# Kernel tuning notes

Measured on AMD Instinct MI355X. Metric: run time of the kernel, lower is better.

Reference implementation:

```python
import jax, jax.numpy as jnp
import numpy as np
import math

IN_CH = 256
EMBED = 128


def setup_inputs() -> dict:
    key = jax.random.key(0)
    k1, k2, k3, k4, k5 = jax.random.split(key, 5)
    N, C, H, W = 4, IN_CH, 64, 64
    x = jax.random.normal(k1, (N, C, H, W), dtype=jnp.float32)
    # conv1x1 weights stored as [out_ch, in_ch] (kernel is 1x1)
    W_qkv = jax.random.normal(k2, (3 * EMBED, C), dtype=jnp.float32) * (1.0 / math.sqrt(C))
    b_qkv = jax.random.normal(k3, (3 * EMBED,), dtype=jnp.float32) * 0.01
    W_out = jax.random.normal(k4, (C, EMBED), dtype=jnp.float32) * (1.0 / math.sqrt(EMBED))
    b_out = jax.random.normal(k5, (C,), dtype=jnp.float32) * 0.01
    return {"x": x, "W_qkv": W_qkv, "b_qkv": b_qkv, "W_out": W_out, "b_out": b_out}


def reference(x, W_qkv, b_qkv, W_out, b_out):
    N, C, H, W = x.shape
    E = EMBED
    HW = H * W
    # conv1x1 QKV projection: (N, 3E, H, W)
    qkv = jnp.einsum('nchw,oc->nohw', x, W_qkv) + b_qkv[None, :, None, None]
    # faithful RAW C-order reshape (N, 3E, H, W) -> (N, HW, 3E), as in torch .reshape
    qkv = qkv.reshape(N, HW, 3 * E)
    q, k, v = jnp.split(qkv, 3, axis=-1)  # each (N, HW, E)
    # scores scaled by 1/sqrt(H*W), softmax over dim=-2 (columns)
    scores = jnp.einsum('nid,njd->nij', q, k) / math.sqrt(HW)
    soft = jax.nn.softmax(scores, axis=-2)
    out = jnp.einsum('nij,njd->nid', soft, v)  # (N, HW, E)
    # faithful RAW C-order reshape (N, HW, E) -> (N, E, H, W)
    out = out.reshape(N, E, H, W)
    # conv1x1 output projection
    y = jnp.einsum('nehw,ce->nchw', out, W_out) + b_out[None, :, None, None]
    return y
```

## Files before the change

kernel.cpp:

```cpp
#include <hip/hip_runtime.h>
#include <hip/hip_bf16.h>


typedef short bfrag __attribute__((ext_vector_type(8)));
typedef float ffrag __attribute__((ext_vector_type(4)));
typedef unsigned short us4 __attribute__((ext_vector_type(4)));
#define MFMA(a,b,c) __builtin_amdgcn_mfma_f32_16x16x32_bf16((a),(b),(c),0,0,0)

__device__ __forceinline__ unsigned short f2bf(float f){
  union { float f; unsigned u; } v; v.f = f;
  unsigned r = v.u + 0x7fffu + ((v.u >> 16) & 1u);
  return (unsigned short)(r >> 16);
}
__device__ __forceinline__ float bf2f(unsigned short h){
  union { unsigned u; float f; } v; v.u = ((unsigned)h) << 16; return v.f;
}
__device__ __forceinline__ unsigned bfpack(float a, float b){
  return (unsigned)f2bf(a) | ((unsigned)f2bf(b) << 16);
}

__global__ __launch_bounds__(256) void k_wcast(const float* __restrict__ Wq, const float* __restrict__ Wo,
                                               unsigned short* __restrict__ Wqb, unsigned short* __restrict__ Wob){
  int i = blockIdx.x*256 + threadIdx.x;
  if (i < 384*256) Wqb[i] = f2bf(Wq[i]);
  if (i < 256*128) Wob[i] = f2bf(Wo[i]);
}

__global__ __launch_bounds__(256) void k_qkv(const float* __restrict__ x, const unsigned short* __restrict__ Wqb,
                                             const float* __restrict__ bq, unsigned short* __restrict__ qkv){
  constexpr int LD = 136;
  __shared__ __align__(16) unsigned short As[64*LD];
  __shared__ __align__(16) unsigned short Bs[64*LD];
  const int o0 = blockIdx.x*64, h0 = blockIdx.y*64, n = blockIdx.z;
  const int t = threadIdx.x, w = t>>6, lane = t&63, lr = lane&15, q4 = lane>>4;
  ffrag acc[4] = {};
  for (int kh = 0; kh < 2; ++kh) {
    __syncthreads();
    #pragma unroll
    for (int r=0;r<4;++r){
      int pi = t + 256*r; int o = pi>>4, seg = pi&15;
      *(uint4*)&As[o*LD + seg*8] = *(const uint4*)(Wqb + (o0+o)*256 + kh*128 + seg*8);
    }
    #pragma unroll
    for (int r=0;r<8;++r){
      int idx = t + 256*r; int cl = idx>>4, h4 = idx&15;
      float4 v = *(const float4*)(x + (size_t)(n*256 + kh*128 + cl)*4096 + h0 + h4*4);
      Bs[(h4*4+0)*LD + cl] = f2bf(v.x);
      Bs[(h4*4+1)*LD + cl] = f2bf(v.y);
      Bs[(h4*4+2)*LD + cl] = f2bf(v.z);
      Bs[(h4*4+3)*LD + cl] = f2bf(v.w);
    }
    __syncthreads();
    #pragma unroll
    for (int kk=0;kk<4;++kk){
      bfrag a = *(const bfrag*)&Bs[(w*16+lr)*LD + kk*32 + q4*8];
      #pragma unroll
      for (int ot=0;ot<4;++ot){
        bfrag b = *(const bfrag*)&As[(ot*16+lr)*LD + kk*32 + q4*8];
        acc[ot] = MFMA(a,b,acc[ot]);
      }
    }
  }
  size_t base = (size_t)n*384*4096;
  #pragma unroll
  for (int ot=0;ot<4;++ot){
    int o  = o0 + ot*16 + lr;
    float bias = bq[o];
    int hw = h0 + w*16 + q4*4;
    us4 pk;
    pk.x = f2bf(acc[ot][0] + bias); pk.y = f2bf(acc[ot][1] + bias);
    pk.z = f2bf(acc[ot][2] + bias); pk.w = f2bf(acc[ot][3] + bias);
    *(us4*)(qkv + base + (size_t)o*4096 + hw) = pk;
  }
}

__global__ __launch_bounds__(256) void k_vtrans(const unsigned short* __restrict__ qkv, unsigned short* __restrict__ vt){
  constexpr int LD = 136;
  __shared__ __align__(16) unsigned short T[64*LD];
  const int p0 = blockIdx.x*64, n = blockIdx.y;
  const int t = threadIdx.x;
  size_t base = (size_t)n*384*4096;
  #pragma unroll
  for (int r=0;r<4;++r){
    int pi = t + 256*r; int pl = pi>>4, seg = pi&15;
    *(uint4*)&T[pl*LD + seg*8] = *(const uint4*)(qkv + base + (size_t)(p0+pl)*384 + 256 + seg*8);
  }
  __syncthreads();
  unsigned* vt32 = (unsigned*)(vt + (size_t)n*128*4096);
  #pragma unroll
  for (int r=0;r<16;++r){
    int pi = t + 256*r;
    int d = pi>>5, k = pi&31;
    unsigned lo = T[(2*k)*LD + d];
    unsigned hi = T[(2*k+1)*LD + d];
    vt32[(size_t)d*2048 + (p0>>1) + k] = lo | (hi<<16);
  }
}

__global__ __launch_bounds__(256) void k_stats(const unsigned short* __restrict__ qkv,
                                               float* __restrict__ zp){
  constexpr int LD = 136;
  __shared__ __align__(16) unsigned short Qs[64*LD];
  const int j0 = blockIdx.x*256, ic = blockIdx.y, n = blockIdx.z;
  const int t = threadIdx.x, w = t>>6, lane = t&63, lr = lane&15, q4 = lane>>4;
  size_t base = (size_t)n*384*4096;
  bfrag kf[4][4];
  #pragma unroll
  for (int js=0; js<4; ++js){
    const unsigned short* krow = qkv + base + (size_t)(j0 + w*64 + js*16 + lr)*384 + 128;
    #pragma unroll
    for (int kk=0;kk<4;++kk) kf[js][kk] = *(const bfrag*)(krow + kk*32 + q4*8);
  }
  float Zc[16] = {};
  const float inv64 = 0.015625f;
  for (int rnd=0; rnd<8; ++rnd){
    int i0 = (ic<<9) + rnd*64;
    __syncthreads();
    #pragma unroll
    for (int r=0;r<4;++r){
      int pi = t + 256*r; int il = pi>>4, seg = pi&15;
      *(uint4*)&Qs[il*LD + seg*8] = *(const uint4*)(qkv + base + (size_t)(i0+il)*384 + seg*8);
    }
    __syncthreads();
    #pragma unroll
    for (int it=0; it<4; ++it){
      bfrag qb[4];
      #pragma unroll
      for (int kk=0;kk<4;++kk) qb[kk] = *(const bfrag*)&Qs[(it*16+lr)*LD + kk*32 + q4*8];
      #pragma unroll
      for (int js=0; js<4; ++js){
        ffrag s = {};
        #pragma unroll
        for (int kk=0;kk<4;++kk) s = MFMA(kf[js][kk], qb[kk], s);
        #pragma unroll
        for (int r=0;r<4;++r) Zc[js*4+r] += __expf(s[r]*inv64);
      }
    }
  }
  #pragma unroll
  for (int v=0; v<16; ++v){
    float z = Zc[v];
    z += __shfl_xor(z, 1); z += __shfl_xor(z, 2);
    z += __shfl_xor(z, 4); z += __shfl_xor(z, 8);
    Zc[v] = z;
  }
  if (lr == 0){
    int jb = j0 + w*64;
    float* zrow = zp + (size_t)((n<<3)+ic)*4096;
    #pragma unroll
    for (int js=0; js<4; ++js)
      #pragma unroll
      for (int r=0;r<4;++r)
        zrow[jb + js*16 + q4*4 + r] = Zc[js*4+r];
  }
}

__global__ __launch_bounds__(256) void k_merge(const float* __restrict__ zp, float* __restrict__ lse){
  int idx = blockIdx.x*256 + threadIdx.x;
  int n = idx>>12, j = idx&4095;
  float Z = 0.f;
  #pragma unroll
  for (int c=0;c<8;++c) Z += zp[(size_t)((n<<3)+c)*4096 + j];
  lse[idx] = __logf(Z);
}

__global__ __launch_bounds__(256) void k_attn(const unsigned short* __restrict__ qkv,
                                              const unsigned short* __restrict__ vtg_all,
                                              const float* __restrict__ lse,
                                              unsigned short* __restrict__ part){
  constexpr int LDK = 136, LDV = 72, LDP = 72;
  __shared__ __align__(16) unsigned short Ks[64*LDK];
  __shared__ __align__(16) unsigned short Vt[128*LDV];
  __shared__ __align__(16) unsigned short Pw[4][32*LDP];
  __shared__ float Ls[64];
  const int i0 = blockIdx.x*128, jh = blockIdx.y, n = blockIdx.z;
  const int t = threadIdx.x, w = t>>6, lane = t&63, lr = lane&15, q4 = lane>>4;
  size_t base = (size_t)n*384*4096;
  const unsigned short* vtg = vtg_all + (size_t)n*128*4096;
  const float* lsen = lse + (n<<12);
  bfrag qf[2][4];
  #pragma unroll
  for (int isub=0;isub<2;++isub){
    const unsigned short* qrow = qkv + base + (size_t)(i0 + w*32 + isub*16 + lr)*384;
    #pragma unroll
    for (int kk=0;kk<4;++kk) qf[isub][kk] = *(const bfrag*)(qrow + kk*32 + q4*8);
  }
  ffrag acc[8][2] = {};
  const float inv64 = 0.015625f;
  for (int j0 = jh*1024; j0 < jh*1024+1024; j0 += 64){
    __syncthreads();
    #pragma unroll
    for (int r=0;r<4;++r){
      int pi = t + 256*r; int jl = pi>>4, seg = pi&15;
      *(uint4*)&Ks[jl*LDK + seg*8] = *(const uint4*)(qkv + base + (size_t)(j0+jl)*384 + 128 + seg*8);
    }
    #pragma unroll
    for (int r=0;r<4;++r){
      int pi = t + 256*r; int d = pi>>3, c = pi&7;
      *(uint4*)&Vt[d*LDV + c*8] = *(const uint4*)(vtg + (size_t)d*4096 + j0 + c*8);
    }
    if (t < 64) Ls[t] = lsen[j0 + t];
    __syncthreads();
    #pragma unroll
    for (int jt=0;jt<4;++jt){
      bfrag kf[4];
      #pragma unroll
      for (int kk=0;kk<4;++kk) kf[kk] = *(const bfrag*)&Ks[(jt*16+lr)*LDK + kk*32 + q4*8];
      float4 l4 = *(const float4*)&Ls[jt*16 + q4*4];
      #pragma unroll
      for (int isub=0;isub<2;++isub){
        ffrag s = {};
        #pragma unroll
        for (int kk=0;kk<4;++kk) s = MFMA(kf[kk], qf[isub][kk], s);
        float p0 = __expf(s[0]*inv64 - l4.x);
        float p1 = __expf(s[1]*inv64 - l4.y);
        float p2 = __expf(s[2]*inv64 - l4.z);
        float p3 = __expf(s[3]*inv64 - l4.w);
        uint2 pk; pk.x = bfpack(p0,p1); pk.y = bfpack(p2,p3);
        *(uint2*)&Pw[w][(isub*16+lr)*LDP + jt*16 + q4*4] = pk;
      }
    }
    asm volatile("" ::: "memory");
    #pragma unroll
    for (int jk=0;jk<2;++jk){
      bfrag pf0 = *(const bfrag*)&Pw[w][lr*LDP      + jk*32 + q4*8];
      bfrag pf1 = *(const bfrag*)&Pw[w][(16+lr)*LDP + jk*32 + q4*8];
      #pragma unroll
      for (int dt=0;dt<8;++dt){
        bfrag af = *(const bfrag*)&Vt[(dt*16+lr)*LDV + jk*32 + q4*8];
        acc[dt][0] = MFMA(af, pf0, acc[dt][0]);
        acc[dt][1] = MFMA(af, pf1, acc[dt][1]);
      }
    }
  }
  unsigned short* po = part + (size_t)(jh*4+n)*524288;
  #pragma unroll
  for (int isub=0;isub<2;++isub){
    const int i = i0 + w*32 + isub*16 + lr;
    #pragma unroll
    for (int dt=0;dt<8;++dt){
      us4 pk;
      pk.x = f2bf(acc[dt][isub][0]); pk.y = f2bf(acc[dt][isub][1]);
      pk.z = f2bf(acc[dt][isub][2]); pk.w = f2bf(acc[dt][isub][3]);
      *(us4*)(po + (size_t)i*128 + dt*16 + q4*4) = pk;
    }
  }
}

__global__ __launch_bounds__(256) void k_oproj(const unsigned short* __restrict__ part,
                                               const unsigned short* __restrict__ Wob,
                                               const float* __restrict__ bo, float* __restrict__ y){
  constexpr int LD = 136;
  __shared__ __align__(16) unsigned short As[128*LD];
  __shared__ __align__(16) unsigned short Rt[64*LD];
  const int c0 = blockIdx.x*128, h0 = blockIdx.y*64, n = blockIdx.z;
  const int t = threadIdx.x, w = t>>6, lane = t&63, lr = lane&15, q4 = lane>>4;
  #pragma unroll
  for (int r=0;r<8;++r){
    int pi = t + 256*r; int cl = pi>>4, seg = pi&15;
    *(uint4*)&As[cl*LD + seg*8] = *(const uint4*)(Wob + (c0+cl)*128 + seg*8);
  }
  #pragma unroll
  for (int r=0;r<8;++r){
    int pi = t + 256*r; int e = pi>>4, h4 = pi&15;
    size_t f = (size_t)e*4096 + h0 + h4*4;
    float a0=0.f,a1=0.f,a2=0.f,a3=0.f;
    #pragma unroll
    for (int s=0;s<4;++s){
      uint2 u = *(const uint2*)(part + (size_t)(s*4+n)*524288 + f);
      a0 += bf2f((unsigned short)(u.x & 0xffffu));
      a1 += bf2f((unsigned short)(u.x >> 16));
      a2 += bf2f((unsigned short)(u.y & 0xffffu));
      a3 += bf2f((unsigned short)(u.y >> 16));
    }
    Rt[(h4*4+0)*LD + e] = f2bf(a0);
    Rt[(h4*4+1)*LD + e] = f2bf(a1);
    Rt[(h4*4+2)*LD + e] = f2bf(a2);
    Rt[(h4*4+3)*LD + e] = f2bf(a3);
  }
  __syncthreads();
  ffrag acc[8] = {};
  #pragma unroll
  for (int kk=0;kk<4;++kk){
    bfrag a = *(const bfrag*)&Rt[(w*16+lr)*LD + kk*32 + q4*8];
    #pragma unroll
    for (int cs=0;cs<8;++cs){
      bfrag b = *(const bfrag*)&As[(cs*16+lr)*LD + kk*32 + q4*8];
      acc[cs] = MFMA(a,b,acc[cs]);
    }
  }
  #pragma unroll
  for (int cs=0;cs<8;++cs){
    int c = c0 + cs*16 + lr;
    float bias = bo[c];
    float4 v4 = { acc[cs][0]+bias, acc[cs][1]+bias, acc[cs][2]+bias, acc[cs][3]+bias };
    *(float4*)(y + ((size_t)n*256 + c)*4096 + h0 + w*16 + q4*4) = v4;
  }
}

extern "C" void kernel_launch(void* const* d_in, const int* in_sizes, int n_in,
                              void* d_out, int out_size, void* d_ws, size_t ws_size,
                              hipStream_t stream){
  const float* x  = (const float*)d_in[0];
  const float* Wq = (const float*)d_in[1];
  const float* bq = (const float*)d_in[2];
  const float* Wo = (const float*)d_in[3];
  const float* bo = (const float*)d_in[4];
  float* y = (float*)d_out;
  char* ws = (char*)d_ws;
  unsigned short* qkv  = (unsigned short*)(ws + 0);
  unsigned short* vtg  = (unsigned short*)(ws + 12582912);
  unsigned short* Wqb  = (unsigned short*)(ws + 16777216);
  unsigned short* Wob  = (unsigned short*)(ws + 16973824);
  float* zp   = (float*)(ws + 17039360);
  float* lse  = (float*)(ws + 17563648);
  unsigned short* part = (unsigned short*)(ws + 17629184);

  k_wcast <<<dim3(384),     256, 0, stream>>>(Wq, Wo, Wqb, Wob);
  k_qkv   <<<dim3(6,64,4),  256, 0, stream>>>(x, Wqb, bq, qkv);
  k_vtrans<<<dim3(64,4),    256, 0, stream>>>(qkv, vtg);
  k_stats <<<dim3(16,8,4),  256, 0, stream>>>(qkv, zp);
  k_merge <<<dim3(64),      256, 0, stream>>>(zp, lse);
  k_attn  <<<dim3(32,4,4),  256, 0, stream>>>(qkv, vtg, lse, part);
  k_oproj <<<dim3(2,64,4),  256, 0, stream>>>(part, Wob, bo, y);
}
```

Baseline: 186.6 us.

## Fuse lse merge into V transpose, widen QKV output tile, vectorize partial loads

Folds the log-sum-exp merge into the V-transpose kernel and moves that kernel after the stats pass, which removes one launch. The QKV projection block now covers 128 output channels instead of 64, so each x tile is converted and reused across twice as many outputs with half the blocks. The output projection reads partial sums as 16-byte loads instead of 8-byte ones. The trade-off is more accumulators and LDS per QKV block, which could lower occupancy, and fewer blocks in that grid.

```diff
diff --git a/kernel.cpp b/kernel.cpp
--- a/kernel.cpp
+++ b/kernel.cpp
@@ -29,15 +29,15 @@
 __global__ __launch_bounds__(256) void k_qkv(const float* __restrict__ x, const unsigned short* __restrict__ Wqb,
                                              const float* __restrict__ bq, unsigned short* __restrict__ qkv){
   constexpr int LD = 136;
-  __shared__ __align__(16) unsigned short As[64*LD];
+  __shared__ __align__(16) unsigned short As[128*LD];
   __shared__ __align__(16) unsigned short Bs[64*LD];
-  const int o0 = blockIdx.x*64, h0 = blockIdx.y*64, n = blockIdx.z;
+  const int o0 = blockIdx.x*128, h0 = blockIdx.y*64, n = blockIdx.z;
   const int t = threadIdx.x, w = t>>6, lane = t&63, lr = lane&15, q4 = lane>>4;
-  ffrag acc[4] = {};
+  ffrag acc[8] = {};
   for (int kh = 0; kh < 2; ++kh) {
     __syncthreads();
     #pragma unroll
-    for (int r=0;r<4;++r){
+    for (int r=0;r<8;++r){
       int pi = t + 256*r; int o = pi>>4, seg = pi&15;
       *(uint4*)&As[o*LD + seg*8] = *(const uint4*)(Wqb + (o0+o)*256 + kh*128 + seg*8);
     }
@@ -55,7 +55,7 @@
     for (int kk=0;kk<4;++kk){
       bfrag a = *(const bfrag*)&Bs[(w*16+lr)*LD + kk*32 + q4*8];
       #pragma unroll
-      for (int ot=0;ot<4;++ot){
+      for (int ot=0;ot<8;++ot){
         bfrag b = *(const bfrag*)&As[(ot*16+lr)*LD + kk*32 + q4*8];
         acc[ot] = MFMA(a,b,acc[ot]);
       }
@@ -63,7 +63,7 @@
   }
   size_t base = (size_t)n*384*4096;
   #pragma unroll
-  for (int ot=0;ot<4;++ot){
+  for (int ot=0;ot<8;++ot){
     int o  = o0 + ot*16 + lr;
     float bias = bq[o];
     int hw = h0 + w*16 + q4*4;
@@ -71,29 +71,6 @@
     pk.x = f2bf(acc[ot][0] + bias); pk.y = f2bf(acc[ot][1] + bias);
     pk.z = f2bf(acc[ot][2] + bias); pk.w = f2bf(acc[ot][3] + bias);
     *(us4*)(qkv + base + (size_t)o*4096 + hw) = pk;
-  }
-}
-
-__global__ __launch_bounds__(256) void k_vtrans(const unsigned short* __restrict__ qkv, unsigned short* __restrict__ vt){
-  constexpr int LD = 136;
-  __shared__ __align__(16) unsigned short T[64*LD];
-  const int p0 = blockIdx.x*64, n = blockIdx.y;
-  const int t = threadIdx.x;
-  size_t base = (size_t)n*384*4096;
-  #pragma unroll
-  for (int r=0;r<4;++r){
-    int pi = t + 256*r; int pl = pi>>4, seg = pi&15;
-    *(uint4*)&T[pl*LD + seg*8] = *(const uint4*)(qkv + base + (size_t)(p0+pl)*384 + 256 + seg*8);
-  }
-  __syncthreads();
-  unsigned* vt32 = (unsigned*)(vt + (size_t)n*128*4096);
-  #pragma unroll
-  for (int r=0;r<16;++r){
-    int pi = t + 256*r;
-    int d = pi>>5, k = pi&31;
-    unsigned lo = T[(2*k)*LD + d];
-    unsigned hi = T[(2*k+1)*LD + d];
-    vt32[(size_t)d*2048 + (p0>>1) + k] = lo | (hi<<16);
   }
 }
 
@@ -155,13 +132,36 @@
   }
 }
 
-__global__ __launch_bounds__(256) void k_merge(const float* __restrict__ zp, float* __restrict__ lse){
-  int idx = blockIdx.x*256 + threadIdx.x;
-  int n = idx>>12, j = idx&4095;
-  float Z = 0.f;
-  #pragma unroll
-  for (int c=0;c<8;++c) Z += zp[(size_t)((n<<3)+c)*4096 + j];
-  lse[idx] = __logf(Z);
+__global__ __launch_bounds__(256) void k_vtrans(const unsigned short* __restrict__ qkv,
+                                                const float* __restrict__ zp,
+                                                unsigned short* __restrict__ vt,
+                                                float* __restrict__ lse){
+  constexpr int LD = 136;
+  __shared__ __align__(16) unsigned short T[64*LD];
+  const int p0 = blockIdx.x*64, n = blockIdx.y;
+  const int t = threadIdx.x;
+  size_t base = (size_t)n*384*4096;
+  #pragma unroll
+  for (int r=0;r<4;++r){
+    int pi = t + 256*r; int pl = pi>>4, seg = pi&15;
+    *(uint4*)&T[pl*LD + seg*8] = *(const uint4*)(qkv + base + (size_t)(p0+pl)*384 + 256 + seg*8);
+  }
+  if (t < 64){
+    float Z = 0.f;
+    #pragma unroll
+    for (int c=0;c<8;++c) Z += zp[(size_t)((n<<3)+c)*4096 + p0 + t];
+    lse[(n<<12) + p0 + t] = __logf(Z);
+  }
+  __syncthreads();
+  unsigned* vt32 = (unsigned*)(vt + (size_t)n*128*4096);
+  #pragma unroll
+  for (int r=0;r<16;++r){
+    int pi = t + 256*r;
+    int d = pi>>5, k = pi&31;
+    unsigned lo = T[(2*k)*LD + d];
+    unsigned hi = T[(2*k+1)*LD + d];
+    vt32[(size_t)d*2048 + (p0>>1) + k] = lo | (hi<<16);
+  }
 }
 
 __global__ __launch_bounds__(256) void k_attn(const unsigned short* __restrict__ qkv,
@@ -261,22 +261,20 @@
     *(uint4*)&As[cl*LD + seg*8] = *(const uint4*)(Wob + (c0+cl)*128 + seg*8);
   }
   #pragma unroll
-  for (int r=0;r<8;++r){
-    int pi = t + 256*r; int e = pi>>4, h4 = pi&15;
-    size_t f = (size_t)e*4096 + h0 + h4*4;
-    float a0=0.f,a1=0.f,a2=0.f,a3=0.f;
+  for (int r=0;r<4;++r){
+    int pi = t + 256*r; int e = pi>>3, h8 = pi&7;
+    size_t f = (size_t)e*4096 + h0 + h8*8;
+    float a[8] = {};
     #pragma unroll
     for (int s=0;s<4;++s){
-      uint2 u = *(const uint2*)(part + (size_t)(s*4+n)*524288 + f);
-      a0 += bf2f((unsigned short)(u.x & 0xffffu));
-      a1 += bf2f((unsigned short)(u.x >> 16));
-      a2 += bf2f((unsigned short)(u.y & 0xffffu));
-      a3 += bf2f((unsigned short)(u.y >> 16));
-    }
-    Rt[(h4*4+0)*LD + e] = f2bf(a0);
-    Rt[(h4*4+1)*LD + e] = f2bf(a1);
-    Rt[(h4*4+2)*LD + e] = f2bf(a2);
-    Rt[(h4*4+3)*LD + e] = f2bf(a3);
+      uint4 u = *(const uint4*)(part + (size_t)(s*4+n)*524288 + f);
+      a[0] += bf2f((unsigned short)(u.x & 0xffffu)); a[1] += bf2f((unsigned short)(u.x >> 16));
+      a[2] += bf2f((unsigned short)(u.y & 0xffffu)); a[3] += bf2f((unsigned short)(u.y >> 16));
+      a[4] += bf2f((unsigned short)(u.z & 0xffffu)); a[5] += bf2f((unsigned short)(u.z >> 16));
+      a[6] += bf2f((unsigned short)(u.w & 0xffffu)); a[7] += bf2f((unsigned short)(u.w >> 16));
+    }
+    #pragma unroll
+    for (int k=0;k<8;++k) Rt[(h8*8+k)*LD + e] = f2bf(a[k]);
   }
   __syncthreads();
   ffrag acc[8] = {};
@@ -317,10 +315,9 @@
   unsigned short* part = (unsigned short*)(ws + 17629184);
 
   k_wcast <<<dim3(384),     256, 0, stream>>>(Wq, Wo, Wqb, Wob);
-  k_qkv   <<<dim3(6,64,4),  256, 0, stream>>>(x, Wqb, bq, qkv);
-  k_vtrans<<<dim3(64,4),    256, 0, stream>>>(qkv, vtg);
+  k_qkv   <<<dim3(3,64,4),  256, 0, stream>>>(x, Wqb, bq, qkv);
   k_stats <<<dim3(16,8,4),  256, 0, stream>>>(qkv, zp);
-  k_merge <<<dim3(64),      256, 0, stream>>>(zp, lse);
+  k_vtrans<<<dim3(64,4),    256, 0, stream>>>(qkv, zp, vtg, lse);
   k_attn  <<<dim3(32,4,4),  256, 0, stream>>>(qkv, vtg, lse, part);
   k_oproj <<<dim3(2,64,4),  256, 0, stream>>>(part, Wob, bo, y);
 }
```

Result: faster. 181.5 us (-2.7%).
